# Kernel tuning notes

Measured on AMD Instinct MI355X. Metric: run time of the kernel, lower is better.

Reference implementation:

```python
import jax, jax.numpy as jnp
import numpy as np

EPS = 1e-8

def layernorm(x, g, b):
    mu = jnp.mean(x, axis=-1, keepdims=True)
    var = jnp.mean((x - mu) ** 2, axis=-1, keepdims=True)
    return (x - mu) * jax.lax.rsqrt(var + EPS) * g + b

def setup_inputs() -> dict:
    key = jax.random.key(0)
    ks = jax.random.split(key, 8)
    B, L, H, V = 512, 201, 128, 100001  # V = item_num + 1
    s = 0.02
    return {
        "input_seqs": jax.random.randint(ks[0], (B, L), 0, V),
        "negs": jax.random.randint(ks[1], (B, L), 0, V),
        # item_emb: torch Linear(V, H, bias=False) weight has shape [H, V]
        "emb_W": jax.random.normal(ks[2], (H, V), dtype=jnp.float32) * s,
        # standard GRU cell params (torch GRUCell layout: [3H, H], gate order r,z,n)
        "Wih": jax.random.normal(ks[3], (3 * H, H), dtype=jnp.float32) * s,
        "Whh": jax.random.normal(ks[4], (3 * H, H), dtype=jnp.float32) * s,
        "bih": jnp.zeros((3 * H,), dtype=jnp.float32),
        "bhh": jnp.zeros((3 * H,), dtype=jnp.float32),
        "ln1_g": jnp.ones((H,), dtype=jnp.float32),
        "ln1_b": jnp.zeros((H,), dtype=jnp.float32),
        "ln2_g": jnp.ones((H,), dtype=jnp.float32),
        "ln2_b": jnp.zeros((H,), dtype=jnp.float32),
    }

def gru_seq(x, Wih, Whh, bih, bhh):
    # x: [B, T, H] -> hidden states [B, T, H]
    B, T, H = x.shape
    # precompute input-side gates once (one big GEMM)
    gi = jnp.einsum('bth,gh->btg', x, Wih) + bih  # [B, T, 3H]
    gi = jnp.moveaxis(gi, 1, 0)                    # [T, B, 3H]

    def step(h, gi_t):
        gh = h @ Whh.T + bhh                       # [B, 3H]
        i_r, i_z, i_n = jnp.split(gi_t, 3, axis=-1)
        h_r, h_z, h_n = jnp.split(gh, 3, axis=-1)
        r = jax.nn.sigmoid(i_r + h_r)
        z = jax.nn.sigmoid(i_z + h_z)
        n = jnp.tanh(i_n + r * h_n)
        h_new = (1.0 - z) * n + z * h
        return h_new, h_new

    h0 = jnp.zeros((B, H), dtype=x.dtype)
    _, hs = jax.lax.scan(step, h0, gi)
    return jnp.moveaxis(hs, 0, 1)                  # [B, T, H]

def reference(input_seqs, negs, emb_W, Wih, Whh, bih, bhh, ln1_g, ln1_b, ln2_g, ln2_b):
    seqs = input_seqs[:, :-1]
    pos = input_seqs[:, 1:]
    neg = negs[:, 1:]
    # F.one_hot(idx, V) @ Linear(V,H) weight^T  ==  gather of emb_W columns
    emb = emb_W.T                                  # [V, H]
    seqs_feats = emb[seqs]                         # [B, T, H]
    pos_feats = emb[pos]
    neg_feats = emb[neg]
    # dropout p=0 -> identity
    seqs_feats = layernorm(seqs_feats, ln1_g, ln1_b)
    logits = gru_seq(seqs_feats, Wih, Whh, bih, bhh)
    logits = layernorm(logits, ln2_g, ln2_b)
    pos_logits = jnp.sum(logits * pos_feats, axis=-1)
    neg_logits = jnp.sum(logits * neg_feats, axis=-1)
    return (pos_logits, neg_logits)
```

## Files before the change

### kernel.cpp

```cpp
#include <hip/hip_runtime.h>

typedef unsigned int u32;
typedef unsigned short u16;
typedef __attribute__((ext_vector_type(8))) short bf16x8;
typedef __attribute__((ext_vector_type(4))) float f32x4;

#define B_   512
#define L_   201
#define T_   200
#define H_   128
#define V_   100001
#define G3_  384
#define M_   (B_*T_)
#define GPB  16
#define NBLK (B_/GPB)
#define HS   136

#define OFF_EMBT 256
#define OFF_GI   25600768ull
#define OFF_HSEQ 104243968ull

__device__ __forceinline__ float bf2f(u16 a) {
    return __uint_as_float(((u32)a) << 16);
}
__device__ __forceinline__ void bf2x2(u32 p, float& lo, float& hi) {
    lo = __uint_as_float(p << 16);
    hi = __uint_as_float(p & 0xffff0000u);
}
__device__ __forceinline__ u16 f2bf(float f) {
    u32 u = __float_as_uint(f);
    u32 lsb = (u >> 16) & 1u;
    u += 0x7fffu + lsb;
    return (u16)(u >> 16);
}
__device__ __forceinline__ u32 packbf(float a, float b) {
#if __has_builtin(__builtin_amdgcn_cvt_pk_bf16_f32)
    typedef __attribute__((ext_vector_type(2))) __bf16 bf16x2_t;
    bf16x2_t r = __builtin_amdgcn_cvt_pk_bf16_f32(a, b);
    return *(u32*)&r;
#else
    return (u32)f2bf(a) | ((u32)f2bf(b) << 16);
#endif
}
__device__ __forceinline__ float frcp(float x) {
    return __builtin_amdgcn_rcpf(x);
}
__device__ __forceinline__ float sigmoidf_(float x) {
    return frcp(1.0f + __expf(-x));
}
__device__ __forceinline__ float tanhf_(float x) {
    return fmaf(-2.0f, frcp(__expf(2.0f * x) + 1.0f), 1.0f);
}
__device__ __forceinline__ void halfred2(float& a, float& b) {
    #pragma unroll
    for (int o = 1; o <= 16; o <<= 1) {
        a += __shfl_xor(a, o, 64);
        b += __shfl_xor(b, o, 64);
    }
}
__device__ __forceinline__ float ldv(const void* p, int dt, int i) {
    return dt ? ((const float*)p)[i] : bf2f(((const u16*)p)[i]);
}
__device__ __forceinline__ void ldsbar() {
    asm volatile("s_waitcnt lgkmcnt(0)\n\ts_barrier" ::: "memory");
}
__device__ __forceinline__ bf16x8 load_frag(const void* W, int dt, int row, int koff) {
    union { bf16x8 v; u32 uu[4]; uint4 q; } r;
    if (dt) {
        const float4* p = (const float4*)((const float*)W + (size_t)row * H_ + koff);
        const float4 a = p[0], b = p[1];
        r.uu[0] = packbf(a.x, a.y); r.uu[1] = packbf(a.z, a.w);
        r.uu[2] = packbf(b.x, b.y); r.uu[3] = packbf(b.z, b.w);
    } else {
        r.q = *(const uint4*)((const u16*)W + (size_t)row * H_ + koff);
    }
    return r.v;
}
#define MFMA16(a, b, c) __builtin_amdgcn_mfma_f32_16x16x32_bf16((a), (b), (c), 0, 0, 0)

__global__ __launch_bounds__(64) void k_sniff(const u32* __restrict__ raw,
                                              int* __restrict__ flag) {
    const int lane = threadIdx.x;
    int big = 0;
    #pragma unroll
    for (int i = 0; i < 16; i++) {
        const u32 w = raw[lane * 16 + i];
        float lo, hi; bf2x2(w, lo, hi);
        if (!(fabsf(lo) <= 16.0f)) big++;
        if (!(fabsf(hi) <= 16.0f)) big++;
    }
    #pragma unroll
    for (int o = 32; o >= 1; o <<= 1) big += __shfl_xor(big, o, 64);
    if (lane == 0) *flag = (big > 8) ? 1 : 0;
}

__global__ __launch_bounds__(1024) void k_transpose(const void* __restrict__ embW,
                                                    u16* __restrict__ embT,
                                                    const int* __restrict__ flag) {
    const int dt = *flag;
    __shared__ u16 tile[32][33];
    const int v0 = blockIdx.x * 32;
    const int h0 = blockIdx.y * 32;
    const int tx = threadIdx.x, ty = threadIdx.y;
    const int v = v0 + tx, h = h0 + ty;
    if (v < V_) {
        u16 val;
        if (dt) val = f2bf(((const float*)embW)[(size_t)h * V_ + v]);
        else    val = ((const u16*)embW)[(size_t)h * V_ + v];
        tile[ty][tx] = val;
    }
    __syncthreads();
    const int vo = v0 + ty, ho = h0 + tx;
    if (vo < V_) embT[(size_t)vo * H_ + ho] = tile[tx][ty];
}

__global__ __launch_bounds__(256) void k_gi(const int* __restrict__ seqs,
                                            const u16* __restrict__ embT,
                                            const void* __restrict__ g1,
                                            const void* __restrict__ b1,
                                            const void* __restrict__ Wih,
                                            const void* __restrict__ bih,
                                            u16* __restrict__ gi2,
                                            const int* __restrict__ flag) {
    const int dt = *flag;
    __shared__ u16 xs[64 * HS];
    const int tid = threadIdx.x;
    const int w = tid >> 6, L = tid & 63;
    const int q = L >> 4, u = L & 15;
    const int lk = L & 31;
    const int hw = w * 2 + (L >> 5);
    const int grp = blockIdx.x / 50;
    const int tc  = blockIdx.x % 50;
    float g1v[4], b1v[4];
    #pragma unroll
    for (int j = 0; j < 4; j++) {
        g1v[j] = ldv(g1, dt, lk * 4 + j);
        b1v[j] = ldv(b1, dt, lk * 4 + j);
    }
    #pragma unroll
    for (int it = 0; it < 8; it++) {
        const int row = hw * 8 + it;
        const int s = row >> 4, bi = row & 15;
        const int b = grp * GPB + bi;
        const int t = tc * 4 + s;
        const int tok = seqs[b * L_ + t];
        const uint2 e = *(const uint2*)&embT[(size_t)tok * H_ + lk * 4];
        float f0, f1, f2, f3; bf2x2(e.x, f0, f1); bf2x2(e.y, f2, f3);
        float s1 = (f0 + f1) + (f2 + f3);
        float s2 = (f0*f0 + f1*f1) + (f2*f2 + f3*f3);
        halfred2(s1, s2);
        const float mu = s1 * (1.0f / H_);
        const float rs = rsqrtf(s2 * (1.0f / H_) - mu * mu + 1e-8f);
        uint2 xw;
        xw.x = packbf((f0-mu)*rs*g1v[0]+b1v[0], (f1-mu)*rs*g1v[1]+b1v[1]);
        xw.y = packbf((f2-mu)*rs*g1v[2]+b1v[2], (f3-mu)*rs*g1v[3]+b1v[3]);
        *(uint2*)&xs[row * HS + lk * 4] = xw;
    }
    bf16x8 af[6][4];
    float bb[6][4];
    #pragma unroll
    for (int j = 0; j < 6; j++) {
        const int nt = w * 6 + j;
        #pragma unroll
        for (int c = 0; c < 4; c++)
            af[j][c] = load_frag(Wih, dt, nt * 16 + u, c * 32 + q * 8);
        if (dt) {
            const float4 bv = *(const float4*)((const float*)bih + nt * 16 + q * 4);
            bb[j][0] = bv.x; bb[j][1] = bv.y; bb[j][2] = bv.z; bb[j][3] = bv.w;
        } else {
            const uint2 bv = *(const uint2*)((const u16*)bih + nt * 16 + q * 4);
            bf2x2(bv.x, bb[j][0], bb[j][1]); bf2x2(bv.y, bb[j][2], bb[j][3]);
        }
    }
    ldsbar();
    #pragma unroll
    for (int s = 0; s < 4; s++) {
        bf16x8 xbv[4];
        #pragma unroll
        for (int c = 0; c < 4; c++)
            xbv[c] = *(const bf16x8*)&xs[(s * 16 + u) * HS + c * 32 + q * 8];
        const int t = tc * 4 + s;
        const size_t base_t = (size_t)(grp * T_ + t) * 6144 + q * 64 + u * 4;
        #pragma unroll
        for (int j = 0; j < 6; j++) {
            const int nt = w * 6 + j;
            f32x4 C = {0.f, 0.f, 0.f, 0.f};
            #pragma unroll
            for (int c = 0; c < 4; c++) C = MFMA16(af[j][c], xbv[c], C);
            uint2 o;
            o.x = packbf(C[0] + bb[j][0], C[1] + bb[j][1]);
            o.y = packbf(C[2] + bb[j][2], C[3] + bb[j][3]);
            *(uint2*)&gi2[base_t + (nt >> 3) * 2048 + (nt & 7) * 256] = o;
        }
    }
}

__global__ __launch_bounds__(512, 2) void k_rec(const u16* __restrict__ gi2,
                                                const void* __restrict__ Whh,
                                                const void* __restrict__ bhh,
                                                u16* __restrict__ hseq2,
                                                const int* __restrict__ flag) {
    const int dt = *flag;
    __shared__ u16 hbuf[2][GPB * HS];
    const int tid = threadIdx.x;
    const int w = tid >> 6, L = tid & 63;
    const int q = L >> 4, u = L & 15;
    const int grp = blockIdx.x;
    for (int i = tid; i < GPB * HS; i += 512) hbuf[0][i] = 0;
    bf16x8 wa[12];
    #pragma unroll
    for (int g = 0; g < 3; g++)
        #pragma unroll
        for (int c = 0; c < 4; c++)
            wa[g * 4 + c] = load_frag(Whh, dt, g * H_ + w * 16 + u, c * 32 + q * 8);
    f32x4 sbr, sbz, sbn;
    #pragma unroll
    for (int r = 0; r < 4; r++) {
        const int i = w * 16 + q * 4 + r;
        sbr[r] = ldv(bhh, dt, i);
        sbz[r] = ldv(bhh, dt, H_ + i);
        sbn[r] = ldv(bhh, dt, 2 * H_ + i);
    }
    float hst[4] = {0.f, 0.f, 0.f, 0.f};
    const u16* gp = gi2 + (size_t)grp * T_ * 6144 + (size_t)w * 256 + q * 64 + u * 4;
    u16* hp = hseq2 + (size_t)grp * T_ * 2048 + (size_t)w * 256 + q * 64 + u * 4;
    uint2 gcur[3], gnxt[3];
    #pragma unroll
    for (int g = 0; g < 3; g++) {
        gcur[g] = *(const uint2*)(gp + 0 * 6144 + g * 2048);
        gnxt[g] = *(const uint2*)(gp + 1 * 6144 + g * 2048);
    }
    ldsbar();
    for (int t = 0; t < T_; t++) {
        const int cur = t & 1;
        const int tpre = (t + 2 < T_) ? (t + 2) : (T_ - 1);
        uint2 g2s[3];
        #pragma unroll
        for (int g = 0; g < 3; g++)
            g2s[g] = *(const uint2*)(gp + (size_t)tpre * 6144 + g * 2048);
        bf16x8 hbv[4];
        #pragma unroll
        for (int c = 0; c < 4; c++)
            hbv[c] = *(const bf16x8*)&hbuf[cur][u * HS + c * 32 + q * 8];
        f32x4 z4 = {0.f, 0.f, 0.f, 0.f};
        f32x4 gr0 = sbr, gr1 = z4, gz0 = sbz, gz1 = z4, gn0 = sbn, gn1 = z4;
        gr0 = MFMA16(wa[0], hbv[0], gr0);  gr0 = MFMA16(wa[1], hbv[1], gr0);
        gr1 = MFMA16(wa[2], hbv[2], gr1);  gr1 = MFMA16(wa[3], hbv[3], gr1);
        gz0 = MFMA16(wa[4], hbv[0], gz0);  gz0 = MFMA16(wa[5], hbv[1], gz0);
        gz1 = MFMA16(wa[6], hbv[2], gz1);  gz1 = MFMA16(wa[7], hbv[3], gz1);
        gn0 = MFMA16(wa[8], hbv[0], gn0);  gn0 = MFMA16(wa[9], hbv[1], gn0);
        gn1 = MFMA16(wa[10], hbv[2], gn1); gn1 = MFMA16(wa[11], hbv[3], gn1);
        float gir[4], giz[4], gin[4];
        bf2x2(gcur[0].x, gir[0], gir[1]); bf2x2(gcur[0].y, gir[2], gir[3]);
        bf2x2(gcur[1].x, giz[0], giz[1]); bf2x2(gcur[1].y, giz[2], giz[3]);
        bf2x2(gcur[2].x, gin[0], gin[1]); bf2x2(gcur[2].y, gin[2], gin[3]);
        float hpv[4];
        #pragma unroll
        for (int r = 0; r < 4; r++) {
            const float rr = sigmoidf_(gir[r] + (gr0[r] + gr1[r]));
            const float zz = sigmoidf_(giz[r] + (gz0[r] + gz1[r]));
            const float nn = tanhf_(fmaf(rr, gn0[r] + gn1[r], gin[r]));
            const float hn = fmaf(zz, hst[r] - nn, nn);
            hst[r] = hn; hpv[r] = hn;
        }
        uint2 hw2;
        hw2.x = packbf(hpv[0], hpv[1]);
        hw2.y = packbf(hpv[2], hpv[3]);
        *(uint2*)&hbuf[cur ^ 1][u * HS + w * 16 + q * 4] = hw2;
        *(uint2*)(hp + (size_t)t * 2048) = hw2;
        gcur[0] = gnxt[0]; gcur[1] = gnxt[1]; gcur[2] = gnxt[2];
        gnxt[0] = g2s[0];  gnxt[1] = g2s[1];  gnxt[2] = g2s[2];
        ldsbar();
    }
}

__global__ __launch_bounds__(256) void k_dot(const int* __restrict__ seqs,
                                             const int* __restrict__ negs,
                                             const u16* __restrict__ hseq2,
                                             const u16* __restrict__ embT,
                                             const void* __restrict__ g2,
                                             const void* __restrict__ b2,
                                             void* __restrict__ out,
                                             const int* __restrict__ flag) {
    const int dt = *flag;
    const int wid = threadIdx.x >> 6;
    const int L = threadIdx.x & 63;
    const int q = L >> 4, u = L & 15;
    const int grp = blockIdx.x / 50;
    const int t   = (blockIdx.x % 50) * 4 + wid;
    const int b   = grp * GPB + u;
    const u16* hc = hseq2 + (size_t)(grp * T_ + t) * 2048;
    uint2 hv[8];
    #pragma unroll
    for (int j = 0; j < 8; j++)
        hv[j] = *(const uint2*)&hc[j * 256 + L * 4];
    const int ptok = seqs[b * L_ + t + 1];
    const int ntok = negs[b * L_ + t + 1];
    float hf[8][4];
    float s1 = 0.f, s2 = 0.f;
    #pragma unroll
    for (int j = 0; j < 8; j++) {
        float a0, a1, a2, a3;
        bf2x2(hv[j].x, a0, a1); bf2x2(hv[j].y, a2, a3);
        hf[j][0] = a0; hf[j][1] = a1; hf[j][2] = a2; hf[j][3] = a3;
        s1 += (a0 + a1) + (a2 + a3);
        s2 += (a0*a0 + a1*a1) + (a2*a2 + a3*a3);
    }
    s1 += __shfl_xor(s1, 16, 64); s2 += __shfl_xor(s2, 16, 64);
    s1 += __shfl_xor(s1, 32, 64); s2 += __shfl_xor(s2, 32, 64);
    const float mu = s1 * (1.0f / H_);
    const float rs = rsqrtf(s2 * (1.0f / H_) - mu * mu + 1e-8f);
    float pe = 0.f, ne = 0.f;
    #pragma unroll
    for (int j = 0; j < 8; j++) {
        const int io = j * 16 + q * 4;
        float gv0, gv1, gv2, gv3, bv0, bv1, bv2, bv3;
        if (dt) {
            const float4 g = *(const float4*)((const float*)g2 + io);
            const float4 bbv = *(const float4*)((const float*)b2 + io);
            gv0 = g.x; gv1 = g.y; gv2 = g.z; gv3 = g.w;
            bv0 = bbv.x; bv1 = bbv.y; bv2 = bbv.z; bv3 = bbv.w;
        } else {
            const uint2 g = *(const uint2*)((const u16*)g2 + io);
            const uint2 bbv = *(const uint2*)((const u16*)b2 + io);
            bf2x2(g.x, gv0, gv1); bf2x2(g.y, gv2, gv3);
            bf2x2(bbv.x, bv0, bv1); bf2x2(bbv.y, bv2, bv3);
        }
        const uint2 pp = *(const uint2*)&embT[(size_t)ptok * H_ + io];
        const uint2 nn = *(const uint2*)&embT[(size_t)ntok * H_ + io];
        float p0, p1, p2, p3, n0, n1, n2, n3;
        bf2x2(pp.x, p0, p1); bf2x2(pp.y, p2, p3);
        bf2x2(nn.x, n0, n1); bf2x2(nn.y, n2, n3);
        const float lo0 = fmaf((hf[j][0] - mu) * rs, gv0, bv0);
        const float lo1 = fmaf((hf[j][1] - mu) * rs, gv1, bv1);
        const float lo2 = fmaf((hf[j][2] - mu) * rs, gv2, bv2);
        const float lo3 = fmaf((hf[j][3] - mu) * rs, gv3, bv3);
        pe += (lo0*p0 + lo1*p1) + (lo2*p2 + lo3*p3);
        ne += (lo0*n0 + lo1*n1) + (lo2*n2 + lo3*n3);
    }
    pe += __shfl_xor(pe, 16, 64); ne += __shfl_xor(ne, 16, 64);
    pe += __shfl_xor(pe, 32, 64); ne += __shfl_xor(ne, 32, 64);
    if (q == 0) {
        const int m = b * T_ + t;
        if (dt) {
            ((float*)out)[m]      = pe;
            ((float*)out)[M_ + m] = ne;
        } else {
            ((u16*)out)[m]        = f2bf(pe);
            ((u16*)out)[M_ + m]   = f2bf(ne);
        }
    }
}

extern "C" void kernel_launch(void* const* d_in, const int* in_sizes, int n_in,
                              void* d_out, int out_size, void* d_ws, size_t ws_size,
                              hipStream_t stream) {
    const int* seqs = (const int*)d_in[0];
    const int* negs = (const int*)d_in[1];
    const void* embW = d_in[2];
    const void* Wih  = d_in[3];
    const void* Whh  = d_in[4];
    const void* bih  = d_in[5];
    const void* bhh  = d_in[6];
    const void* g1   = d_in[7];
    const void* b1   = d_in[8];
    const void* g2   = d_in[9];
    const void* b2   = d_in[10];

    char* ws = (char*)d_ws;
    int* flag = (int*)ws;
    u16* embT  = (u16*)(ws + OFF_EMBT);
    u16* gi2   = (u16*)(ws + OFF_GI);
    u16* hseq2 = (u16*)(ws + OFF_HSEQ);

    k_sniff<<<1, 64, 0, stream>>>((const u32*)embW, flag);
    k_transpose<<<dim3((V_ + 31) / 32, H_ / 32), dim3(32, 32), 0, stream>>>(embW, embT, flag);
    k_gi<<<M_ / 64, 256, 0, stream>>>(seqs, embT, g1, b1, Wih, bih, gi2, flag);
    k_rec<<<NBLK, 512, 0, stream>>>(gi2, Whh, bhh, hseq2, flag);
    k_dot<<<M_ / 64, 256, 0, stream>>>(seqs, negs, hseq2, embT, g2, b2, d_out, flag);
}
```

Before: 358.1 us.

## Halve batch per recurrent block, fold biases and exp2 scaling into input gates

```diff
diff --git a/kernel.cpp b/kernel.cpp
--- a/kernel.cpp
+++ b/kernel.cpp
@@ -13,12 +13,16 @@
 #define G3_  384
 #define M_   (B_*T_)
 #define GPB  16
-#define NBLK (B_/GPB)
+#define RB   8
+#define NBLK8 (B_/RB)
 #define HS   136
 
 #define OFF_EMBT 256
 #define OFF_GI   25600768ull
 #define OFF_HSEQ 104243968ull
+
+#define S_RZ (-1.44269504088896340736f)
+#define S_N  ( 2.88539008177792681472f)
 
 __device__ __forceinline__ float bf2f(u16 a) {
     return __uint_as_float(((u32)a) << 16);
@@ -45,11 +49,12 @@
 __device__ __forceinline__ float frcp(float x) {
     return __builtin_amdgcn_rcpf(x);
 }
-__device__ __forceinline__ float sigmoidf_(float x) {
-    return frcp(1.0f + __expf(-x));
-}
-__device__ __forceinline__ float tanhf_(float x) {
-    return fmaf(-2.0f, frcp(__expf(2.0f * x) + 1.0f), 1.0f);
+__device__ __forceinline__ float fexp2(float x) {
+#if __has_builtin(__builtin_amdgcn_exp2f)
+    return __builtin_amdgcn_exp2f(x);
+#else
+    return exp2f(x);
+#endif
 }
 __device__ __forceinline__ void halfred2(float& a, float& b) {
     #pragma unroll
@@ -120,7 +125,8 @@
                                             const void* __restrict__ b1,
                                             const void* __restrict__ Wih,
                                             const void* __restrict__ bih,
-                                            u16* __restrict__ gi2,
+                                            const void* __restrict__ bhh,
+                                            u32* __restrict__ gi2,
                                             const int* __restrict__ flag) {
     const int dt = *flag;
     __shared__ u16 xs[64 * HS];
@@ -157,117 +163,120 @@
         *(uint2*)&xs[row * HS + lk * 4] = xw;
     }
     bf16x8 af[6][4];
-    float bb[6][4];
+    float bS[6], Sj[6];
     #pragma unroll
     for (int j = 0; j < 6; j++) {
         const int nt = w * 6 + j;
         #pragma unroll
         for (int c = 0; c < 4; c++)
             af[j][c] = load_frag(Wih, dt, nt * 16 + u, c * 32 + q * 8);
-        if (dt) {
-            const float4 bv = *(const float4*)((const float*)bih + nt * 16 + q * 4);
-            bb[j][0] = bv.x; bb[j][1] = bv.y; bb[j][2] = bv.z; bb[j][3] = bv.w;
-        } else {
-            const uint2 bv = *(const uint2*)((const u16*)bih + nt * 16 + q * 4);
-            bf2x2(bv.x, bb[j][0], bb[j][1]); bf2x2(bv.y, bb[j][2], bb[j][3]);
-        }
+        const int o = nt * 16 + u;
+        const float S = (nt >= 16) ? S_N : S_RZ;
+        float bias = ldv(bih, dt, o);
+        if (nt < 16) bias += ldv(bhh, dt, o);
+        Sj[j] = S; bS[j] = bias * S;
     }
     ldsbar();
+    const int rgrp = grp * 2 + (q >> 1);
+    const int pb = (q & 1) * 2;
     #pragma unroll
     for (int s = 0; s < 4; s++) {
-        bf16x8 xbv[4];
+        bf16x8 xav[4];
         #pragma unroll
         for (int c = 0; c < 4; c++)
-            xbv[c] = *(const bf16x8*)&xs[(s * 16 + u) * HS + c * 32 + q * 8];
+            xav[c] = *(const bf16x8*)&xs[(s * 16 + u) * HS + c * 32 + q * 8];
         const int t = tc * 4 + s;
-        const size_t base_t = (size_t)(grp * T_ + t) * 6144 + q * 64 + u * 4;
+        u32* sb = gi2 + (size_t)(rgrp * T_ + t) * 1536;
         #pragma unroll
         for (int j = 0; j < 6; j++) {
             const int nt = w * 6 + j;
+            const int g = nt >> 3;
+            const int ih = (nt & 7) * 16 + u;
             f32x4 C = {0.f, 0.f, 0.f, 0.f};
             #pragma unroll
-            for (int c = 0; c < 4; c++) C = MFMA16(af[j][c], xbv[c], C);
-            uint2 o;
-            o.x = packbf(C[0] + bb[j][0], C[1] + bb[j][1]);
-            o.y = packbf(C[2] + bb[j][2], C[3] + bb[j][3]);
-            *(uint2*)&gi2[base_t + (nt >> 3) * 2048 + (nt & 7) * 256] = o;
+            for (int c = 0; c < 4; c++) C = MFMA16(xav[c], af[j][c], C);
+            sb[(pb + 0) * 384 + g * 128 + ih] =
+                packbf(fmaf(C[0], Sj[j], bS[j]), fmaf(C[1], Sj[j], bS[j]));
+            sb[(pb + 1) * 384 + g * 128 + ih] =
+                packbf(fmaf(C[2], Sj[j], bS[j]), fmaf(C[3], Sj[j], bS[j]));
         }
     }
 }
 
-__global__ __launch_bounds__(512, 2) void k_rec(const u16* __restrict__ gi2,
+__global__ __launch_bounds__(512, 2) void k_rec(const u32* __restrict__ gi2,
                                                 const void* __restrict__ Whh,
                                                 const void* __restrict__ bhh,
-                                                u16* __restrict__ hseq2,
+                                                u32* __restrict__ hseq2,
                                                 const int* __restrict__ flag) {
     const int dt = *flag;
-    __shared__ u16 hbuf[2][GPB * HS];
+    __shared__ u16 hbuf[2][RB * HS];
     const int tid = threadIdx.x;
     const int w = tid >> 6, L = tid & 63;
     const int q = L >> 4, u = L & 15;
+    const int ub = u & 7;
     const int grp = blockIdx.x;
-    for (int i = tid; i < GPB * HS; i += 512) hbuf[0][i] = 0;
-    bf16x8 wa[12];
+    for (int i = tid; i < RB * HS; i += 512) hbuf[0][i] = 0;
+    bf16x8 wb[12];
     #pragma unroll
     for (int g = 0; g < 3; g++)
         #pragma unroll
         for (int c = 0; c < 4; c++)
-            wa[g * 4 + c] = load_frag(Whh, dt, g * H_ + w * 16 + u, c * 32 + q * 8);
-    f32x4 sbr, sbz, sbn;
-    #pragma unroll
-    for (int r = 0; r < 4; r++) {
-        const int i = w * 16 + q * 4 + r;
-        sbr[r] = ldv(bhh, dt, i);
-        sbz[r] = ldv(bhh, dt, H_ + i);
-        sbn[r] = ldv(bhh, dt, 2 * H_ + i);
-    }
-    float hst[4] = {0.f, 0.f, 0.f, 0.f};
-    const u16* gp = gi2 + (size_t)grp * T_ * 6144 + (size_t)w * 256 + q * 64 + u * 4;
-    u16* hp = hseq2 + (size_t)grp * T_ * 2048 + (size_t)w * 256 + q * 64 + u * 4;
-    uint2 gcur[3], gnxt[3];
+            wb[g * 4 + c] = load_frag(Whh, dt, g * H_ + w * 16 + u, c * 32 + q * 8);
+    const float sbn = ldv(bhh, dt, 2 * H_ + w * 16 + u);
+    const int p  = ((q & 1) << 1) | (q >> 1);
+    const int ih = w * 16 + u;
+    const int hi = q >> 1;
+    const u32* gp = gi2 + (size_t)grp * T_ * 1536 + p * 384 + ih;
+    u32* hp = hseq2 + (size_t)grp * T_ * 512 + p * 128 + ih;
+    u32 gcur[3], gnxt[3];
     #pragma unroll
     for (int g = 0; g < 3; g++) {
-        gcur[g] = *(const uint2*)(gp + 0 * 6144 + g * 2048);
-        gnxt[g] = *(const uint2*)(gp + 1 * 6144 + g * 2048);
-    }
+        gcur[g] = gp[g * 128];
+        gnxt[g] = gp[1536 + g * 128];
+    }
+    float hst0 = 0.f, hst1 = 0.f;
     ldsbar();
+    #pragma unroll 2
     for (int t = 0; t < T_; t++) {
         const int cur = t & 1;
         const int tpre = (t + 2 < T_) ? (t + 2) : (T_ - 1);
-        uint2 g2s[3];
+        u32 g2s[3];
         #pragma unroll
         for (int g = 0; g < 3; g++)
-            g2s[g] = *(const uint2*)(gp + (size_t)tpre * 6144 + g * 2048);
+            g2s[g] = gp[(size_t)tpre * 1536 + g * 128];
         bf16x8 hbv[4];
         #pragma unroll
         for (int c = 0; c < 4; c++)
-            hbv[c] = *(const bf16x8*)&hbuf[cur][u * HS + c * 32 + q * 8];
-        f32x4 z4 = {0.f, 0.f, 0.f, 0.f};
-        f32x4 gr0 = sbr, gr1 = z4, gz0 = sbz, gz1 = z4, gn0 = sbn, gn1 = z4;
-        gr0 = MFMA16(wa[0], hbv[0], gr0);  gr0 = MFMA16(wa[1], hbv[1], gr0);
-        gr1 = MFMA16(wa[2], hbv[2], gr1);  gr1 = MFMA16(wa[3], hbv[3], gr1);
-        gz0 = MFMA16(wa[4], hbv[0], gz0);  gz0 = MFMA16(wa[5], hbv[1], gz0);
-        gz1 = MFMA16(wa[6], hbv[2], gz1);  gz1 = MFMA16(wa[7], hbv[3], gz1);
-        gn0 = MFMA16(wa[8], hbv[0], gn0);  gn0 = MFMA16(wa[9], hbv[1], gn0);
-        gn1 = MFMA16(wa[10], hbv[2], gn1); gn1 = MFMA16(wa[11], hbv[3], gn1);
-        float gir[4], giz[4], gin[4];
-        bf2x2(gcur[0].x, gir[0], gir[1]); bf2x2(gcur[0].y, gir[2], gir[3]);
-        bf2x2(gcur[1].x, giz[0], giz[1]); bf2x2(gcur[1].y, giz[2], giz[3]);
-        bf2x2(gcur[2].x, gin[0], gin[1]); bf2x2(gcur[2].y, gin[2], gin[3]);
-        float hpv[4];
-        #pragma unroll
-        for (int r = 0; r < 4; r++) {
-            const float rr = sigmoidf_(gir[r] + (gr0[r] + gr1[r]));
-            const float zz = sigmoidf_(giz[r] + (gz0[r] + gz1[r]));
-            const float nn = tanhf_(fmaf(rr, gn0[r] + gn1[r], gin[r]));
-            const float hn = fmaf(zz, hst[r] - nn, nn);
-            hst[r] = hn; hpv[r] = hn;
-        }
-        uint2 hw2;
-        hw2.x = packbf(hpv[0], hpv[1]);
-        hw2.y = packbf(hpv[2], hpv[3]);
-        *(uint2*)&hbuf[cur ^ 1][u * HS + w * 16 + q * 4] = hw2;
-        *(uint2*)(hp + (size_t)t * 2048) = hw2;
+            hbv[c] = *(const bf16x8*)&hbuf[cur][ub * HS + c * 32 + q * 8];
+        f32x4 ar = {0.f, 0.f, 0.f, 0.f};
+        f32x4 az = {0.f, 0.f, 0.f, 0.f};
+        f32x4 an = {sbn, sbn, sbn, sbn};
+        #pragma unroll
+        for (int c = 0; c < 4; c++) ar = MFMA16(hbv[c], wb[c], ar);
+        #pragma unroll
+        for (int c = 0; c < 4; c++) az = MFMA16(hbv[c], wb[4 + c], az);
+        #pragma unroll
+        for (int c = 0; c < 4; c++) an = MFMA16(hbv[c], wb[8 + c], an);
+        const float grv0 = hi ? ar[2] : ar[0], grv1 = hi ? ar[3] : ar[1];
+        const float gzv0 = hi ? az[2] : az[0], gzv1 = hi ? az[3] : az[1];
+        const float gnv0 = hi ? an[2] : an[0], gnv1 = hi ? an[3] : an[1];
+        float gir0, gir1, giz0, giz1, gin0, gin1;
+        bf2x2(gcur[0], gir0, gir1);
+        bf2x2(gcur[1], giz0, giz1);
+        bf2x2(gcur[2], gin0, gin1);
+        const float rr0 = frcp(1.0f + fexp2(fmaf(S_RZ, grv0, gir0)));
+        const float zz0 = frcp(1.0f + fexp2(fmaf(S_RZ, gzv0, giz0)));
+        const float nn0 = fmaf(-2.0f, frcp(fexp2(fmaf(rr0 * S_N, gnv0, gin0)) + 1.0f), 1.0f);
+        const float h0 = fmaf(zz0, hst0 - nn0, nn0);
+        const float rr1 = frcp(1.0f + fexp2(fmaf(S_RZ, grv1, gir1)));
+        const float zz1 = frcp(1.0f + fexp2(fmaf(S_RZ, gzv1, giz1)));
+        const float nn1 = fmaf(-2.0f, frcp(fexp2(fmaf(rr1 * S_N, gnv1, gin1)) + 1.0f), 1.0f);
+        const float h1 = fmaf(zz1, hst1 - nn1, nn1);
+        hst0 = h0; hst1 = h1;
+        const u32 hw2 = packbf(h0, h1);
+        hbuf[cur ^ 1][(p * 2) * HS + ih]     = (u16)hw2;
+        hbuf[cur ^ 1][(p * 2 + 1) * HS + ih] = (u16)(hw2 >> 16);
+        hp[(size_t)t * 512] = hw2;
         gcur[0] = gnxt[0]; gcur[1] = gnxt[1]; gcur[2] = gnxt[2];
         gnxt[0] = g2s[0];  gnxt[1] = g2s[1];  gnxt[2] = g2s[2];
         ldsbar();
@@ -276,7 +285,7 @@
 
 __global__ __launch_bounds__(256) void k_dot(const int* __restrict__ seqs,
                                              const int* __restrict__ negs,
-                                             const u16* __restrict__ hseq2,
+                                             const u32* __restrict__ hseq2,
                                              const u16* __restrict__ embT,
                                              const void* __restrict__ g2,
                                              const void* __restrict__ b2,
@@ -286,68 +295,64 @@
     const int wid = threadIdx.x >> 6;
     const int L = threadIdx.x & 63;
     const int q = L >> 4, u = L & 15;
-    const int grp = blockIdx.x / 50;
-    const int t   = (blockIdx.x % 50) * 4 + wid;
-    const int b   = grp * GPB + u;
-    const u16* hc = hseq2 + (size_t)(grp * T_ + t) * 2048;
-    uint2 hv[8];
-    #pragma unroll
-    for (int j = 0; j < 8; j++)
-        hv[j] = *(const uint2*)&hc[j * 256 + L * 4];
-    const int ptok = seqs[b * L_ + t + 1];
-    const int ntok = negs[b * L_ + t + 1];
-    float hf[8][4];
-    float s1 = 0.f, s2 = 0.f;
+    const int idx = blockIdx.x * 4 + wid;
+    const int grp = idx / T_;
+    const int t = idx - grp * T_;
+    const int b0 = grp * 8 + q * 2;
+    const u32* hc = hseq2 + ((size_t)(grp * T_ + t) * 4 + q) * 128 + u * 8;
+    const uint4 ha = *(const uint4*)hc;
+    const uint4 hb = *(const uint4*)(hc + 4);
+    const u32 hv[8] = {ha.x, ha.y, ha.z, ha.w, hb.x, hb.y, hb.z, hb.w};
+    float hlo[8], hhi[8];
+    float s1a = 0.f, s2a = 0.f, s1b = 0.f, s2b = 0.f;
     #pragma unroll
     for (int j = 0; j < 8; j++) {
-        float a0, a1, a2, a3;
-        bf2x2(hv[j].x, a0, a1); bf2x2(hv[j].y, a2, a3);
-        hf[j][0] = a0; hf[j][1] = a1; hf[j][2] = a2; hf[j][3] = a3;
-        s1 += (a0 + a1) + (a2 + a3);
-        s2 += (a0*a0 + a1*a1) + (a2*a2 + a3*a3);
-    }
-    s1 += __shfl_xor(s1, 16, 64); s2 += __shfl_xor(s2, 16, 64);
-    s1 += __shfl_xor(s1, 32, 64); s2 += __shfl_xor(s2, 32, 64);
-    const float mu = s1 * (1.0f / H_);
-    const float rs = rsqrtf(s2 * (1.0f / H_) - mu * mu + 1e-8f);
-    float pe = 0.f, ne = 0.f;
+        float lo, hh; bf2x2(hv[j], lo, hh);
+        hlo[j] = lo; hhi[j] = hh;
+        s1a += lo; s2a += lo * lo;
+        s1b += hh; s2b += hh * hh;
+    }
+    #pragma unroll
+    for (int o = 1; o <= 8; o <<= 1) {
+        s1a += __shfl_xor(s1a, o, 64); s2a += __shfl_xor(s2a, o, 64);
+        s1b += __shfl_xor(s1b, o, 64); s2b += __shfl_xor(s2b, o, 64);
+    }
+    const float mua = s1a * (1.0f / H_);
+    const float rsa = rsqrtf(s2a * (1.0f / H_) - mua * mua + 1e-8f);
+    const float mub = s1b * (1.0f / H_);
+    const float rsb = rsqrtf(s2b * (1.0f / H_) - mub * mub + 1e-8f);
+    const int pt0 = seqs[b0 * L_ + t + 1],       nt0 = negs[b0 * L_ + t + 1];
+    const int pt1 = seqs[(b0 + 1) * L_ + t + 1], nt1 = negs[(b0 + 1) * L_ + t + 1];
+    const bf16x8 P0 = *(const bf16x8*)&embT[(size_t)pt0 * H_ + u * 8];
+    const bf16x8 N0 = *(const bf16x8*)&embT[(size_t)nt0 * H_ + u * 8];
+    const bf16x8 P1 = *(const bf16x8*)&embT[(size_t)pt1 * H_ + u * 8];
+    const bf16x8 N1 = *(const bf16x8*)&embT[(size_t)nt1 * H_ + u * 8];
+    float pe0 = 0.f, ne0 = 0.f, pe1 = 0.f, ne1 = 0.f;
     #pragma unroll
     for (int j = 0; j < 8; j++) {
-        const int io = j * 16 + q * 4;
-        float gv0, gv1, gv2, gv3, bv0, bv1, bv2, bv3;
+        const float gvj = ldv(g2, dt, u * 8 + j);
+        const float bvj = ldv(b2, dt, u * 8 + j);
+        const float la = fmaf((hlo[j] - mua) * rsa, gvj, bvj);
+        const float lb = fmaf((hhi[j] - mub) * rsb, gvj, bvj);
+        pe0 = fmaf(la, bf2f((u16)P0[j]), pe0);
+        ne0 = fmaf(la, bf2f((u16)N0[j]), ne0);
+        pe1 = fmaf(lb, bf2f((u16)P1[j]), pe1);
+        ne1 = fmaf(lb, bf2f((u16)N1[j]), ne1);
+    }
+    #pragma unroll
+    for (int o = 1; o <= 8; o <<= 1) {
+        pe0 += __shfl_xor(pe0, o, 64); ne0 += __shfl_xor(ne0, o, 64);
+        pe1 += __shfl_xor(pe1, o, 64); ne1 += __shfl_xor(ne1, o, 64);
+    }
+    if (u == 0) {
+        const int m0 = b0 * T_ + t;
+        const int m1 = m0 + T_;
         if (dt) {
-            const float4 g = *(const float4*)((const float*)g2 + io);
-            const float4 bbv = *(const float4*)((const float*)b2 + io);
-            gv0 = g.x; gv1 = g.y; gv2 = g.z; gv3 = g.w;
-            bv0 = bbv.x; bv1 = bbv.y; bv2 = bbv.z; bv3 = bbv.w;
+            ((float*)out)[m0] = pe0;      ((float*)out)[M_ + m0] = ne0;
+            ((float*)out)[m1] = pe1;      ((float*)out)[M_ + m1] = ne1;
         } else {
-            const uint2 g = *(const uint2*)((const u16*)g2 + io);
-            const uint2 bbv = *(const uint2*)((const u16*)b2 + io);
-            bf2x2(g.x, gv0, gv1); bf2x2(g.y, gv2, gv3);
-            bf2x2(bbv.x, bv0, bv1); bf2x2(bbv.y, bv2, bv3);
-        }
-        const uint2 pp = *(const uint2*)&embT[(size_t)ptok * H_ + io];
-        const uint2 nn = *(const uint2*)&embT[(size_t)ntok * H_ + io];
-        float p0, p1, p2, p3, n0, n1, n2, n3;
-        bf2x2(pp.x, p0, p1); bf2x2(pp.y, p2, p3);
-        bf2x2(nn.x, n0, n1); bf2x2(nn.y, n2, n3);
-        const float lo0 = fmaf((hf[j][0] - mu) * rs, gv0, bv0);
-        const float lo1 = fmaf((hf[j][1] - mu) * rs, gv1, bv1);
-        const float lo2 = fmaf((hf[j][2] - mu) * rs, gv2, bv2);
-        const float lo3 = fmaf((hf[j][3] - mu) * rs, gv3, bv3);
-        pe += (lo0*p0 + lo1*p1) + (lo2*p2 + lo3*p3);
-        ne += (lo0*n0 + lo1*n1) + (lo2*n2 + lo3*n3);
-    }
-    pe += __shfl_xor(pe, 16, 64); ne += __shfl_xor(ne, 16, 64);
-    pe += __shfl_xor(pe, 32, 64); ne += __shfl_xor(ne, 32, 64);
-    if (q == 0) {
-        const int m = b * T_ + t;
-        if (dt) {
-            ((float*)out)[m]      = pe;
-            ((float*)out)[M_ + m] = ne;
-        } else {
-            ((u16*)out)[m]        = f2bf(pe);
-            ((u16*)out)[M_ + m]   = f2bf(ne);
+            ((u16*)out)[m0] = f2bf(pe0);  ((u16*)out)[M_ + m0] = f2bf(ne0);
+            ((u16*)out)[m1] = f2bf(pe1);  ((u16*)out)[M_ + m1] = f2bf(ne1);
         }
     }
 }
@@ -370,12 +375,12 @@
     char* ws = (char*)d_ws;
     int* flag = (int*)ws;
     u16* embT  = (u16*)(ws + OFF_EMBT);
-    u16* gi2   = (u16*)(ws + OFF_GI);
-    u16* hseq2 = (u16*)(ws + OFF_HSEQ);
+    u32* gi2   = (u32*)(ws + OFF_GI);
+    u32* hseq2 = (u32*)(ws + OFF_HSEQ);
 
     k_sniff<<<1, 64, 0, stream>>>((const u32*)embW, flag);
     k_transpose<<<dim3((V_ + 31) / 32, H_ / 32), dim3(32, 32), 0, stream>>>(embW, embT, flag);
-    k_gi<<<M_ / 64, 256, 0, stream>>>(seqs, embT, g1, b1, Wih, bih, gi2, flag);
-    k_rec<<<NBLK, 512, 0, stream>>>(gi2, Whh, bhh, hseq2, flag);
-    k_dot<<<M_ / 64, 256, 0, stream>>>(seqs, negs, hseq2, embT, g2, b2, d_out, flag);
-}
+    k_gi<<<M_ / 64, 256, 0, stream>>>(seqs, embT, g1, b1, Wih, bih, bhh, gi2, flag);
+    k_rec<<<NBLK8, 512, 0, stream>>>(gi2, Whh, bhh, hseq2, flag);
+    k_dot<<<(B_ / 8) * T_ / 4, 256, 0, stream>>>(seqs, negs, hseq2, embT, g2, b2, d_out, flag);
+}
```

Measured after the change: 330.7 us. 7.6% less time.
